# Kernel tuning notes

Hardware: AMD Instinct MI355X
Metric: run time of the kernel (lower is better)

Reference implementation:

```python
import jax, jax.numpy as jnp
import numpy as np

EPS = 1e-5

def _ln(x, g, b):
    mu = jnp.mean(x, axis=-1, keepdims=True)
    var = jnp.var(x, axis=-1, keepdims=True)
    return (x - mu) * jax.lax.rsqrt(var + EPS) * g + b

def setup_inputs() -> dict:
    key = jax.random.key(0)
    ks = jax.random.split(key, 8)
    B, N, D, H = 1, 512, 128, 128
    s = 1.0 / np.sqrt(D)
    inp = {
        'x': jax.random.normal(ks[0], (B, N, N, D), dtype=jnp.float32),
        'src_mask': jax.random.randint(ks[1], (B, N), 0, 2, dtype=jnp.int32),
        'ln_g': jnp.ones((D,), jnp.float32), 'ln_b': jnp.zeros((D,), jnp.float32),
        'Wl': jax.random.normal(ks[2], (D, H), jnp.float32) * s,
        'bl': jnp.zeros((H,), jnp.float32),
        'Wr': jax.random.normal(ks[3], (D, H), jnp.float32) * s,
        'br': jnp.zeros((H,), jnp.float32),
        # gates: faithful to nn.init.constant_(weight, 0.), constant_(bias, 1.)
        'Wlg': jnp.zeros((D, H), jnp.float32), 'blg': jnp.ones((H,), jnp.float32),
        'Wrg': jnp.zeros((D, H), jnp.float32), 'brg': jnp.ones((H,), jnp.float32),
        'Wog': jnp.zeros((D, H), jnp.float32), 'bog': jnp.ones((H,), jnp.float32),
        'oln_g': jnp.ones((H,), jnp.float32), 'oln_b': jnp.zeros((H,), jnp.float32),
        'Wo': jax.random.normal(ks[4], (H, D), jnp.float32) / np.sqrt(H),
        'bo': jnp.zeros((D,), jnp.float32),
    }
    return inp

def reference(x, src_mask, ln_g, ln_b, Wl, bl, Wr, br, Wlg, blg, Wrg, brg, Wog, bog, oln_g, oln_b, Wo, bo):
    # pairwise mask (B,i,j,1) = outer product of src_mask with itself
    m = src_mask.astype(jnp.float32)
    mask = (m[:, :, None] * m[:, None, :])[..., None]
    xn = _ln(x, ln_g, ln_b)
    # original applies left/right proj to detached xn (no grad to x via these paths)
    xd = jax.lax.stop_gradient(xn)
    left = (xd @ Wl + bl) * mask
    right = (xd @ Wr + br) * mask
    left = left * jax.nn.sigmoid(xn @ Wlg + blg)
    right = right * jax.nn.sigmoid(xn @ Wrg + brg)
    out_gate = jax.nn.sigmoid(xn @ Wog + bog)
    # ingoing mix: '... k j d, ... k i d -> ... i j d'
    out = jnp.einsum('bkjd,bkid->bijd', left, right)
    out = _ln(out, oln_g, oln_b) * out_gate
    return out @ Wo + bo
```

## Files before the change

kernel.cpp:

```cpp
#include <hip/hip_runtime.h>
#include <stdint.h>

#define NN 512
#define PP (NN * NN)

typedef __attribute__((ext_vector_type(8))) short bf16x8;
typedef __attribute__((ext_vector_type(4))) short bf16x4;
typedef __attribute__((ext_vector_type(4))) float f32x4;

#define MFMA16 __builtin_amdgcn_mfma_f32_16x16x32_bf16

__device__ __forceinline__ unsigned short f2bf(float f) {
  unsigned u = __float_as_uint(f);
  u += 0x7fffu + ((u >> 16) & 1u);
  return (unsigned short)(u >> 16);
}
__device__ __forceinline__ float bf2f(unsigned short s) {
  return __uint_as_float(((unsigned)s) << 16);
}
__device__ __forceinline__ unsigned pack2(float a, float b) {
  return (unsigned)f2bf(a) | ((unsigned)f2bf(b) << 16);
}
__device__ __forceinline__ float sigm(float t) { return 1.0f / (1.0f + __expf(-t)); }

__device__ __forceinline__ int sidx(int p, int h) {
  return p * 136 + (h ^ (((p >> 3) & 7) << 3));
}

__global__ __launch_bounds__(256) void k_prep(
    const float* __restrict__ w0, const float* __restrict__ w1,
    const float* __restrict__ w2, const float* __restrict__ w3,
    const float* __restrict__ w4, const float* __restrict__ w5,
    unsigned short* __restrict__ outw) {
  const float* src;
  switch (blockIdx.x) {
    case 0: src = w0; break; case 1: src = w1; break; case 2: src = w2; break;
    case 3: src = w3; break; case 4: src = w4; break; default: src = w5; break;
  }
  unsigned short* o = outw + blockIdx.x * 16384;
  for (int idx = threadIdx.x; idx < 16384; idx += 256) {
    int r = idx >> 7, c = idx & 127;
    o[idx] = f2bf(src[c * 128 + r]);
  }
}

__global__ __launch_bounds__(256) void k_ln(
    const float* __restrict__ x, const float* __restrict__ g,
    const float* __restrict__ b, unsigned short* __restrict__ xn) {
  const int lane = threadIdx.x & 63, wid = threadIdx.x >> 6;
  const int row = blockIdx.x * 32 + wid * 8 + (lane >> 3);
  const int ch = lane & 7;
  const float4* xr = (const float4*)(x + (size_t)row * 128 + ch * 16);
  float4 V[4];
  float s = 0.f, ss = 0.f;
#pragma unroll
  for (int q = 0; q < 4; ++q) {
    V[q] = xr[q];
    s  += V[q].x + V[q].y + V[q].z + V[q].w;
    ss += V[q].x * V[q].x + V[q].y * V[q].y + V[q].z * V[q].z + V[q].w * V[q].w;
  }
#pragma unroll
  for (int o = 1; o < 8; o <<= 1) { s += __shfl_xor(s, o); ss += __shfl_xor(ss, o); }
  float mu  = s * 0.0078125f;
  float var = ss * 0.0078125f - mu * mu;
  float rs  = rsqrtf(var + 1e-5f);
  const float4* gp = (const float4*)(g + ch * 16);
  const float4* bp = (const float4*)(b + ch * 16);
  unsigned pk[8];
#pragma unroll
  for (int q = 0; q < 4; ++q) {
    float4 vv = V[q], gg = gp[q], bb = bp[q];
    pk[2 * q]     = pack2((vv.x - mu) * rs * gg.x + bb.x, (vv.y - mu) * rs * gg.y + bb.y);
    pk[2 * q + 1] = pack2((vv.z - mu) * rs * gg.z + bb.z, (vv.w - mu) * rs * gg.w + bb.w);
  }
  unsigned short* dst = xn + (size_t)row * 128 + ch * 16;
  *(uint4*)dst       = make_uint4(pk[0], pk[1], pk[2], pk[3]);
  *(uint4*)(dst + 8) = make_uint4(pk[4], pk[5], pk[6], pk[7]);
}

__global__ __launch_bounds__(256) void k_proj(
    const unsigned short* __restrict__ xn,
    const unsigned short* __restrict__ WpT, const float* __restrict__ bp,
    const unsigned short* __restrict__ WgT, const float* __restrict__ bg,
    const int* __restrict__ mask,
    unsigned short* __restrict__ outb) {
  const int c  = blockIdx.y;
  const int k0 = blockIdx.x * 128;
  const int t = threadIdx.x, lane = t & 63, wid = t >> 6;
  const int wm = (wid >> 1) * 64, wn = (wid & 1) * 64;
  const int lr = lane & 15, lg = lane >> 4;
  __shared__ unsigned short sX[128 * 136];
  __shared__ unsigned short sW[128 * 136];

#pragma unroll
  for (int it = 0; it < 8; ++it) {
    int lin = it * 256 + t;
    int r = lin >> 4, ch = lin & 15;
    *(uint4*)&sX[r * 136 + ch * 8] =
        *(const uint4*)&xn[((size_t)(k0 + r) * NN + c) * 128 + ch * 8];
  }
#pragma unroll
  for (int it = 0; it < 8; ++it) {
    int lin = it * 256 + t;
    *(uint4*)&sW[(lin >> 4) * 136 + (lin & 15) * 8] = *(const uint4*)&WgT[lin * 8];
  }
  __syncthreads();

  f32x4 acc[4][4];
#pragma unroll
  for (int m = 0; m < 4; ++m)
#pragma unroll
    for (int n = 0; n < 4; ++n) { acc[m][n][0] = 0.f; acc[m][n][1] = 0.f; acc[m][n][2] = 0.f; acc[m][n][3] = 0.f; }

#pragma unroll
  for (int kk = 0; kk < 4; ++kk) {
    bf16x8 av[4], bv[4];
#pragma unroll
    for (int m = 0; m < 4; ++m)
      av[m] = *(const bf16x8*)&sW[(wm + m * 16 + lr) * 136 + kk * 32 + lg * 8];
#pragma unroll
    for (int n = 0; n < 4; ++n)
      bv[n] = *(const bf16x8*)&sX[(wn + n * 16 + lr) * 136 + kk * 32 + lg * 8];
#pragma unroll
    for (int m = 0; m < 4; ++m)
#pragma unroll
      for (int n = 0; n < 4; ++n)
        acc[m][n] = MFMA16(av[m], bv[n], acc[m][n], 0, 0, 0);
  }
  float sg[4][4][4];
#pragma unroll
  for (int m = 0; m < 4; ++m)
#pragma unroll
    for (int r = 0; r < 4; ++r) {
      int h = wm + m * 16 + lg * 4 + r;
      float bgv = bg[h];
#pragma unroll
      for (int n = 0; n < 4; ++n) sg[m][n][r] = sigm(acc[m][n][r] + bgv);
    }
  __syncthreads();
#pragma unroll
  for (int it = 0; it < 8; ++it) {
    int lin = it * 256 + t;
    *(uint4*)&sW[(lin >> 4) * 136 + (lin & 15) * 8] = *(const uint4*)&WpT[lin * 8];
  }
  __syncthreads();

#pragma unroll
  for (int m = 0; m < 4; ++m)
#pragma unroll
    for (int n = 0; n < 4; ++n) { acc[m][n][0] = 0.f; acc[m][n][1] = 0.f; acc[m][n][2] = 0.f; acc[m][n][3] = 0.f; }
#pragma unroll
  for (int kk = 0; kk < 4; ++kk) {
    bf16x8 av[4], bv[4];
#pragma unroll
    for (int m = 0; m < 4; ++m)
      av[m] = *(const bf16x8*)&sW[(wm + m * 16 + lr) * 136 + kk * 32 + lg * 8];
#pragma unroll
    for (int n = 0; n < 4; ++n)
      bv[n] = *(const bf16x8*)&sX[(wn + n * 16 + lr) * 136 + kk * 32 + lg * 8];
#pragma unroll
    for (int m = 0; m < 4; ++m)
#pragma unroll
      for (int n = 0; n < 4; ++n)
        acc[m][n] = MFMA16(av[m], bv[n], acc[m][n], 0, 0, 0);
  }

  const int maskc = mask[c];
  float mcol[4];
#pragma unroll
  for (int n = 0; n < 4; ++n)
    mcol[n] = (float)(maskc * mask[k0 + wn + n * 16 + lr]);
#pragma unroll
  for (int m = 0; m < 4; ++m)
#pragma unroll
    for (int r = 0; r < 4; ++r) {
      int h = wm + m * 16 + lg * 4 + r;
      float bpv = bp[h];
#pragma unroll
      for (int n = 0; n < 4; ++n) {
        float v = (acc[m][n][r] + bpv) * mcol[n] * sg[m][n][r];
        outb[(size_t)h * PP + (size_t)c * NN + k0 + wn + n * 16 + lr] = f2bf(v);
      }
    }
}

__global__ __launch_bounds__(512) void k_einsum(
    const unsigned short* __restrict__ rightT,
    const unsigned short* __restrict__ leftT,
    unsigned short* __restrict__ tmp) {
  const int bid = (blockIdx.x & 7) * 64 + (blockIdx.x >> 3);
  const int d = bid >> 2;
  const int i0 = ((bid >> 1) & 1) * 256, j0 = (bid & 1) * 256;
  const unsigned short* A = rightT + (size_t)d * PP;
  const unsigned short* B = leftT + (size_t)d * PP;
  const int t = threadIdx.x, lane = t & 63, wid = t >> 6;
  const int wm = (wid >> 2) * 128, wn = (wid & 3) * 64;
  const int lr = lane & 15, lg = lane >> 4;
  __shared__ unsigned short sA[256 * 72];
  __shared__ unsigned short sB[256 * 72];

  f32x4 acc[8][4];
#pragma unroll
  for (int m = 0; m < 8; ++m)
#pragma unroll
    for (int n = 0; n < 4; ++n) { acc[m][n][0] = 0.f; acc[m][n][1] = 0.f; acc[m][n][2] = 0.f; acc[m][n][3] = 0.f; }

  for (int kb = 0; kb < 8; ++kb) {
#pragma unroll
    for (int it = 0; it < 4; ++it) {
      int lin = it * 512 + t;
      int r = lin >> 3, ch = lin & 7;
      *(uint4*)&sA[r * 72 + ch * 8] =
          *(const uint4*)&A[(size_t)(i0 + r) * NN + kb * 64 + ch * 8];
      *(uint4*)&sB[r * 72 + ch * 8] =
          *(const uint4*)&B[(size_t)(j0 + r) * NN + kb * 64 + ch * 8];
    }
    __syncthreads();
#pragma unroll
    for (int kk = 0; kk < 2; ++kk) {
      bf16x8 bv[4];
#pragma unroll
      for (int n = 0; n < 4; ++n)
        bv[n] = *(const bf16x8*)&sB[(wn + n * 16 + lr) * 72 + kk * 32 + lg * 8];
#pragma unroll
      for (int m = 0; m < 8; ++m) {
        bf16x8 av = *(const bf16x8*)&sA[(wm + m * 16 + lr) * 72 + kk * 32 + lg * 8];
#pragma unroll
        for (int n = 0; n < 4; ++n)
          acc[m][n] = MFMA16(av, bv[n], acc[m][n], 0, 0, 0);
      }
    }
    __syncthreads();
  }
#pragma unroll
  for (int m = 0; m < 8; ++m)
#pragma unroll
    for (int r = 0; r < 4; ++r) {
      int row = wm + m * 16 + lg * 4 + r;
#pragma unroll
      for (int n = 0; n < 4; ++n) {
        int col = wn + n * 16 + lr;
        tmp[(size_t)d * PP + (size_t)(i0 + row) * NN + j0 + col] = f2bf(acc[m][n][r]);
      }
    }
}

__global__ __launch_bounds__(512, 4) void k_final(
    const unsigned short* __restrict__ xn,
    const unsigned short* __restrict__ WogT, const float* __restrict__ bog,
    const unsigned short* __restrict__ WoT, const float* __restrict__ bo,
    const unsigned short* __restrict__ tmp,
    const float* __restrict__ og, const float* __restrict__ ob,
    float* __restrict__ out) {
  const int p0 = blockIdx.x * 128;
  const int t = threadIdx.x, lane = t & 63, wid = t >> 6;
  const int wm = (wid >> 2) * 64, wn = (wid & 3) * 32;
  const int lr = lane & 15, lg = lane >> 4;
  __shared__ unsigned short sT[128 * 136];
  __shared__ unsigned short sSig[128 * 136];

  {
    const int ps = t & 15;
    const int hb = ((t >> 4) & 15) * 8 + (t >> 8) * 4;
    uint4 a[4];
#pragma unroll
    for (int e = 0; e < 4; ++e)
      a[e] = *(const uint4*)&tmp[(size_t)(hb + e) * PP + p0 + 8 * ps];
#pragma unroll
    for (int r = 0; r < 8; ++r) {
      bf16x4 y;
#pragma unroll
      for (int e = 0; e < 4; ++e) {
        unsigned w = ((const unsigned*)&a[e])[r >> 1];
        y[e] = (short)((r & 1) ? (w >> 16) : (w & 0xffffu));
      }
      *(bf16x4*)&sT[sidx(8 * ps + r, hb)] = y;
    }
  }

  f32x4 acc[4][2];
#pragma unroll
  for (int m = 0; m < 4; ++m)
#pragma unroll
    for (int n = 0; n < 2; ++n) { acc[m][n][0] = 0.f; acc[m][n][1] = 0.f; acc[m][n][2] = 0.f; acc[m][n][3] = 0.f; }
#pragma unroll
  for (int kk = 0; kk < 4; ++kk) {
    bf16x8 av[4], bv[2];
#pragma unroll
    for (int m = 0; m < 4; ++m)
      av[m] = *(const bf16x8*)&xn[(size_t)(p0 + wm + m * 16 + lr) * 128 + kk * 32 + lg * 8];
#pragma unroll
    for (int n = 0; n < 2; ++n)
      bv[n] = *(const bf16x8*)&WogT[(wn + n * 16 + lr) * 128 + kk * 32 + lg * 8];
#pragma unroll
    for (int m = 0; m < 4; ++m)
#pragma unroll
      for (int n = 0; n < 2; ++n)
        acc[m][n] = MFMA16(av[m], bv[n], acc[m][n], 0, 0, 0);
  }
  float bogv[2];
#pragma unroll
  for (int n = 0; n < 2; ++n) bogv[n] = bog[wn + n * 16 + lr];
#pragma unroll
  for (int m = 0; m < 4; ++m)
#pragma unroll
    for (int r = 0; r < 4; ++r) {
      int p = wm + m * 16 + lg * 4 + r;
#pragma unroll
      for (int n = 0; n < 2; ++n)
        sSig[sidx(p, wn + n * 16 + lr)] = f2bf(sigm(acc[m][n][r] + bogv[n]));
    }
  __syncthreads();

  {
    const int p = t >> 2, q = t & 3;
    bf16x8 tv[4];
    float s = 0.f, ss = 0.f;
#pragma unroll
    for (int c = 0; c < 4; ++c) {
      tv[c] = *(const bf16x8*)&sT[sidx(p, q * 32 + c * 8)];
#pragma unroll
      for (int e = 0; e < 8; ++e) {
        float f = bf2f((unsigned short)tv[c][e]);
        s += f; ss += f * f;
      }
    }
    s += __shfl_xor(s, 1); ss += __shfl_xor(ss, 1);
    s += __shfl_xor(s, 2); ss += __shfl_xor(ss, 2);
    float mu = s * 0.0078125f;
    float var = ss * 0.0078125f - mu * mu;
    float rs = rsqrtf(var + 1e-5f);
#pragma unroll
    for (int c = 0; c < 4; ++c) {
      int h0 = q * 32 + c * 8;
      float4 og0 = *(const float4*)&og[h0], og1 = *(const float4*)&og[h0 + 4];
      float4 ob0 = *(const float4*)&ob[h0], ob1 = *(const float4*)&ob[h0 + 4];
      float ogv[8] = {og0.x, og0.y, og0.z, og0.w, og1.x, og1.y, og1.z, og1.w};
      float obv[8] = {ob0.x, ob0.y, ob0.z, ob0.w, ob1.x, ob1.y, ob1.z, ob1.w};
      bf16x8 gv = *(const bf16x8*)&sSig[sidx(p, h0)];
      bf16x8 y;
#pragma unroll
      for (int e = 0; e < 8; ++e) {
        float alpha = rs * ogv[e];
        float beta = fmaf(-mu, alpha, obv[e]);
        float yf = fmaf(bf2f((unsigned short)tv[c][e]), alpha, beta) *
                   bf2f((unsigned short)gv[e]);
        y[e] = (short)f2bf(yf);
      }
      *(bf16x8*)&sT[sidx(p, h0)] = y;
    }
  }
  __syncthreads();

#pragma unroll
  for (int m = 0; m < 4; ++m)
#pragma unroll
    for (int n = 0; n < 2; ++n) { acc[m][n][0] = 0.f; acc[m][n][1] = 0.f; acc[m][n][2] = 0.f; acc[m][n][3] = 0.f; }
#pragma unroll
  for (int kk = 0; kk < 4; ++kk) {
    const int h0 = kk * 32 + lg * 8;
    bf16x8 av[4], bv[2];
#pragma unroll
    for (int m = 0; m < 4; ++m)
      av[m] = *(const bf16x8*)&sT[sidx(wm + m * 16 + lr, h0)];
#pragma unroll
    for (int n = 0; n < 2; ++n)
      bv[n] = *(const bf16x8*)&WoT[(wn + n * 16 + lr) * 128 + h0];
#pragma unroll
    for (int m = 0; m < 4; ++m)
#pragma unroll
      for (int n = 0; n < 2; ++n)
        acc[m][n] = MFMA16(av[m], bv[n], acc[m][n], 0, 0, 0);
  }

  float bov[2];
#pragma unroll
  for (int n = 0; n < 2; ++n) bov[n] = bo[wn + n * 16 + lr];
#pragma unroll
  for (int m = 0; m < 4; ++m)
#pragma unroll
    for (int r = 0; r < 4; ++r) {
      int p = wm + m * 16 + lg * 4 + r;
#pragma unroll
      for (int n = 0; n < 2; ++n)
        out[(size_t)(p0 + p) * 128 + wn + n * 16 + lr] = acc[m][n][r] + bov[n];
    }
}

extern "C" void kernel_launch(void* const* d_in, const int* in_sizes, int n_in,
                              void* d_out, int out_size, void* d_ws, size_t ws_size,
                              hipStream_t stream) {
  (void)in_sizes; (void)n_in; (void)out_size;
  const float* x    = (const float*)d_in[0];
  const int*   msk  = (const int*)d_in[1];
  const float* ln_g = (const float*)d_in[2];
  const float* ln_b = (const float*)d_in[3];
  const float* Wl   = (const float*)d_in[4];
  const float* bl   = (const float*)d_in[5];
  const float* Wr   = (const float*)d_in[6];
  const float* br   = (const float*)d_in[7];
  const float* Wlg  = (const float*)d_in[8];
  const float* blg  = (const float*)d_in[9];
  const float* Wrg  = (const float*)d_in[10];
  const float* brg  = (const float*)d_in[11];
  const float* Wog  = (const float*)d_in[12];
  const float* bog  = (const float*)d_in[13];
  const float* olng = (const float*)d_in[14];
  const float* olnb = (const float*)d_in[15];
  const float* Wo   = (const float*)d_in[16];
  const float* bo   = (const float*)d_in[17];
  float* out = (float*)d_out;

  const size_t need = (1ull << 20) + 4ull * (1ull << 26);
  if (ws_size < need) return;
  char* ws = (char*)d_ws;
  unsigned short* wT    = (unsigned short*)ws;
  unsigned short* xn    = (unsigned short*)(ws + (1ull << 20));
  unsigned short* leftT = (unsigned short*)(ws + (1ull << 20) + (1ull << 26));
  unsigned short* rightT= (unsigned short*)(ws + (1ull << 20) + (2ull << 26));
  unsigned short* tmp   = (unsigned short*)(ws + (1ull << 20) + (3ull << 26));

  hipLaunchKernelGGL(k_prep, dim3(6), dim3(256), 0, stream, Wl, Wr, Wlg, Wrg, Wog, Wo, wT);
  hipLaunchKernelGGL(k_ln, dim3(PP / 32), dim3(256), 0, stream, x, ln_g, ln_b, xn);
  hipLaunchKernelGGL(k_proj, dim3(4, NN), dim3(256), 0, stream,
                     xn, wT + 0 * 16384, bl, wT + 2 * 16384, blg, msk, leftT);
  hipLaunchKernelGGL(k_proj, dim3(4, NN), dim3(256), 0, stream,
                     xn, wT + 1 * 16384, br, wT + 3 * 16384, brg, msk, rightT);
  hipLaunchKernelGGL(k_einsum, dim3(512), dim3(512), 0, stream, rightT, leftT, tmp);
  hipLaunchKernelGGL(k_final, dim3(PP / 128), dim3(512), 0, stream,
                     xn, wT + 4 * 16384, bog, wT + 5 * 16384, bo, tmp, olng, olnb, out);
}
```

Before: 305.7 us.

## Restructure final kernel so each wave owns 16 rows, keeping the gate in registers

Rewrites k_final so each wave owns 16 pair rows across all 128 channels. The out-gate GEMM is computed transposed so the sigmoid values stay in registers, and the LayerNorm, gating and Wo GEMM are fused in registers through cross-lane shuffles. This removes the sSig shared buffer, one __syncthreads and a shared-memory round trip for the normalized activations. Blocks shrink to 64 rows and 256 threads, which raises register pressure and changes occupancy, and the shuffle-based lane remapping is intricate and could be wrong.

```diff
diff --git a/kernel.cpp b/kernel.cpp
--- a/kernel.cpp
+++ b/kernel.cpp
@@ -22,6 +22,15 @@
   return (unsigned)f2bf(a) | ((unsigned)f2bf(b) << 16);
 }
 __device__ __forceinline__ float sigm(float t) { return 1.0f / (1.0f + __expf(-t)); }
+
+__device__ __forceinline__ f32x4 shflx4(f32x4 v, int m) {
+  f32x4 r;
+  r[0] = __shfl_xor(v[0], m);
+  r[1] = __shfl_xor(v[1], m);
+  r[2] = __shfl_xor(v[2], m);
+  r[3] = __shfl_xor(v[3], m);
+  return r;
+}
 
 __device__ __forceinline__ int sidx(int p, int h) {
   return p * 136 + (h ^ (((p >> 3) & 7) << 3));
@@ -245,23 +254,21 @@
     }
 }
 
-__global__ __launch_bounds__(512, 4) void k_final(
+__global__ __launch_bounds__(256, 3) void k_final(
     const unsigned short* __restrict__ xn,
     const unsigned short* __restrict__ WogT, const float* __restrict__ bog,
     const unsigned short* __restrict__ WoT, const float* __restrict__ bo,
     const unsigned short* __restrict__ tmp,
     const float* __restrict__ og, const float* __restrict__ ob,
     float* __restrict__ out) {
-  const int p0 = blockIdx.x * 128;
+  const int p0 = blockIdx.x * 64;
   const int t = threadIdx.x, lane = t & 63, wid = t >> 6;
-  const int wm = (wid >> 2) * 64, wn = (wid & 3) * 32;
   const int lr = lane & 15, lg = lane >> 4;
-  __shared__ unsigned short sT[128 * 136];
-  __shared__ unsigned short sSig[128 * 136];
+  __shared__ unsigned short sT[64 * 136];
 
   {
-    const int ps = t & 15;
-    const int hb = ((t >> 4) & 15) * 8 + (t >> 8) * 4;
+    const int ps = t & 7;
+    const int hb = (t >> 3) * 4;
     uint4 a[4];
 #pragma unroll
     for (int e = 0; e < 4; ++e)
@@ -278,113 +285,96 @@
     }
   }
 
-  f32x4 acc[4][2];
-#pragma unroll
-  for (int m = 0; m < 4; ++m)
-#pragma unroll
-    for (int n = 0; n < 2; ++n) { acc[m][n][0] = 0.f; acc[m][n][1] = 0.f; acc[m][n][2] = 0.f; acc[m][n][3] = 0.f; }
+  const int prow = p0 + wid * 16 + lr;
+
+  f32x4 acc1[8];
+#pragma unroll
+  for (int m = 0; m < 8; ++m) { acc1[m][0] = 0.f; acc1[m][1] = 0.f; acc1[m][2] = 0.f; acc1[m][3] = 0.f; }
 #pragma unroll
   for (int kk = 0; kk < 4; ++kk) {
-    bf16x8 av[4], bv[2];
-#pragma unroll
-    for (int m = 0; m < 4; ++m)
-      av[m] = *(const bf16x8*)&xn[(size_t)(p0 + wm + m * 16 + lr) * 128 + kk * 32 + lg * 8];
-#pragma unroll
-    for (int n = 0; n < 2; ++n)
-      bv[n] = *(const bf16x8*)&WogT[(wn + n * 16 + lr) * 128 + kk * 32 + lg * 8];
-#pragma unroll
-    for (int m = 0; m < 4; ++m)
-#pragma unroll
-      for (int n = 0; n < 2; ++n)
-        acc[m][n] = MFMA16(av[m], bv[n], acc[m][n], 0, 0, 0);
-  }
-  float bogv[2];
-#pragma unroll
-  for (int n = 0; n < 2; ++n) bogv[n] = bog[wn + n * 16 + lr];
-#pragma unroll
-  for (int m = 0; m < 4; ++m)
+    bf16x8 bvx = *(const bf16x8*)&xn[(size_t)prow * 128 + kk * 32 + lg * 8];
+#pragma unroll
+    for (int m = 0; m < 8; ++m) {
+      bf16x8 av = *(const bf16x8*)&WogT[(m * 16 + lr) * 128 + kk * 32 + lg * 8];
+      acc1[m] = MFMA16(av, bvx, acc1[m], 0, 0, 0);
+    }
+  }
+  f32x4 sigv[8];
+#pragma unroll
+  for (int m = 0; m < 8; ++m) {
+    float4 b4 = *(const float4*)&bog[m * 16 + lg * 4];
+    sigv[m][0] = sigm(acc1[m][0] + b4.x);
+    sigv[m][1] = sigm(acc1[m][1] + b4.y);
+    sigv[m][2] = sigm(acc1[m][2] + b4.z);
+    sigv[m][3] = sigm(acc1[m][3] + b4.w);
+  }
+
+  __syncthreads();
+
+  bf16x8 tv[4];
+  float s = 0.f, ss = 0.f;
+#pragma unroll
+  for (int kk = 0; kk < 4; ++kk) {
+    tv[kk] = *(const bf16x8*)&sT[sidx(wid * 16 + lr, kk * 32 + lg * 8)];
+#pragma unroll
+    for (int e = 0; e < 8; ++e) {
+      float f = bf2f((unsigned short)tv[kk][e]);
+      s += f; ss += f * f;
+    }
+  }
+  s += __shfl_xor(s, 16); ss += __shfl_xor(ss, 16);
+  s += __shfl_xor(s, 32); ss += __shfl_xor(ss, 32);
+  const float mu = s * 0.0078125f;
+  const float rs = rsqrtf(ss * 0.0078125f - mu * mu + 1e-5f);
+
+  f32x4 acc2[8];
+#pragma unroll
+  for (int n = 0; n < 8; ++n) { acc2[n][0] = 0.f; acc2[n][1] = 0.f; acc2[n][2] = 0.f; acc2[n][3] = 0.f; }
+#pragma unroll
+  for (int kk = 0; kk < 4; ++kk) {
+    f32x4 w1 = (lg & 2) ? sigv[2 * kk + 1] : sigv[2 * kk];
+    f32x4 w2 = (lg & 2) ? sigv[2 * kk] : sigv[2 * kk + 1];
+    f32x4 r16 = shflx4(w1, 16);
+    f32x4 r32 = shflx4(w2, 32);
+    f32x4 r48 = shflx4(w2, 48);
+    f32x4 h0v = (lg == 0) ? sigv[2 * kk]
+              : (lg == 1) ? r48
+              : (lg == 2) ? r32 : r16;
+    f32x4 h1v = (lg == 3) ? sigv[2 * kk + 1]
+              : (lg == 0) ? r16
+              : (lg == 1) ? r32 : r48;
+
+    const int h0 = kk * 32 + lg * 8;
+    float4 og0 = *(const float4*)&og[h0], og1 = *(const float4*)&og[h0 + 4];
+    float4 ob0 = *(const float4*)&ob[h0], ob1 = *(const float4*)&ob[h0 + 4];
+    float ogv[8] = {og0.x, og0.y, og0.z, og0.w, og1.x, og1.y, og1.z, og1.w};
+    float obv[8] = {ob0.x, ob0.y, ob0.z, ob0.w, ob1.x, ob1.y, ob1.z, ob1.w};
+    float sgv[8] = {h0v[0], h0v[1], h0v[2], h0v[3], h1v[0], h1v[1], h1v[2], h1v[3]};
+
+    bf16x8 yv;
+#pragma unroll
+    for (int e = 0; e < 8; ++e) {
+      float alpha = rs * ogv[e];
+      float beta = fmaf(-mu, alpha, obv[e]);
+      float yf = fmaf(bf2f((unsigned short)tv[kk][e]), alpha, beta) * sgv[e];
+      yv[e] = (short)f2bf(yf);
+    }
+#pragma unroll
+    for (int n = 0; n < 8; ++n) {
+      bf16x8 bv = *(const bf16x8*)&WoT[(n * 16 + lr) * 128 + h0];
+      acc2[n] = MFMA16(yv, bv, acc2[n], 0, 0, 0);
+    }
+  }
+
+#pragma unroll
+  for (int n = 0; n < 8; ++n) {
+    float bov = bo[n * 16 + lr];
 #pragma unroll
     for (int r = 0; r < 4; ++r) {
-      int p = wm + m * 16 + lg * 4 + r;
-#pragma unroll
-      for (int n = 0; n < 2; ++n)
-        sSig[sidx(p, wn + n * 16 + lr)] = f2bf(sigm(acc[m][n][r] + bogv[n]));
-    }
-  __syncthreads();
-
-  {
-    const int p = t >> 2, q = t & 3;
-    bf16x8 tv[4];
-    float s = 0.f, ss = 0.f;
-#pragma unroll
-    for (int c = 0; c < 4; ++c) {
-      tv[c] = *(const bf16x8*)&sT[sidx(p, q * 32 + c * 8)];
-#pragma unroll
-      for (int e = 0; e < 8; ++e) {
-        float f = bf2f((unsigned short)tv[c][e]);
-        s += f; ss += f * f;
-      }
-    }
-    s += __shfl_xor(s, 1); ss += __shfl_xor(ss, 1);
-    s += __shfl_xor(s, 2); ss += __shfl_xor(ss, 2);
-    float mu = s * 0.0078125f;
-    float var = ss * 0.0078125f - mu * mu;
-    float rs = rsqrtf(var + 1e-5f);
-#pragma unroll
-    for (int c = 0; c < 4; ++c) {
-      int h0 = q * 32 + c * 8;
-      float4 og0 = *(const float4*)&og[h0], og1 = *(const float4*)&og[h0 + 4];
-      float4 ob0 = *(const float4*)&ob[h0], ob1 = *(const float4*)&ob[h0 + 4];
-      float ogv[8] = {og0.x, og0.y, og0.z, og0.w, og1.x, og1.y, og1.z, og1.w};
-      float obv[8] = {ob0.x, ob0.y, ob0.z, ob0.w, ob1.x, ob1.y, ob1.z, ob1.w};
-      bf16x8 gv = *(const bf16x8*)&sSig[sidx(p, h0)];
-      bf16x8 y;
-#pragma unroll
-      for (int e = 0; e < 8; ++e) {
-        float alpha = rs * ogv[e];
-        float beta = fmaf(-mu, alpha, obv[e]);
-        float yf = fmaf(bf2f((unsigned short)tv[c][e]), alpha, beta) *
-                   bf2f((unsigned short)gv[e]);
-        y[e] = (short)f2bf(yf);
-      }
-      *(bf16x8*)&sT[sidx(p, h0)] = y;
-    }
-  }
-  __syncthreads();
-
-#pragma unroll
-  for (int m = 0; m < 4; ++m)
-#pragma unroll
-    for (int n = 0; n < 2; ++n) { acc[m][n][0] = 0.f; acc[m][n][1] = 0.f; acc[m][n][2] = 0.f; acc[m][n][3] = 0.f; }
-#pragma unroll
-  for (int kk = 0; kk < 4; ++kk) {
-    const int h0 = kk * 32 + lg * 8;
-    bf16x8 av[4], bv[2];
-#pragma unroll
-    for (int m = 0; m < 4; ++m)
-      av[m] = *(const bf16x8*)&sT[sidx(wm + m * 16 + lr, h0)];
-#pragma unroll
-    for (int n = 0; n < 2; ++n)
-      bv[n] = *(const bf16x8*)&WoT[(wn + n * 16 + lr) * 128 + h0];
-#pragma unroll
-    for (int m = 0; m < 4; ++m)
-#pragma unroll
-      for (int n = 0; n < 2; ++n)
-        acc[m][n] = MFMA16(av[m], bv[n], acc[m][n], 0, 0, 0);
-  }
-
-  float bov[2];
-#pragma unroll
-  for (int n = 0; n < 2; ++n) bov[n] = bo[wn + n * 16 + lr];
-#pragma unroll
-  for (int m = 0; m < 4; ++m)
-#pragma unroll
-    for (int r = 0; r < 4; ++r) {
-      int p = wm + m * 16 + lg * 4 + r;
-#pragma unroll
-      for (int n = 0; n < 2; ++n)
-        out[(size_t)(p0 + p) * 128 + wn + n * 16 + lr] = acc[m][n][r] + bov[n];
-    }
+      int p = p0 + wid * 16 + lg * 4 + r;
+      out[(size_t)p * 128 + n * 16 + lr] = acc2[n][r] + bov;
+    }
+  }
 }
 
 extern "C" void kernel_launch(void* const* d_in, const int* in_sizes, int n_in,
@@ -427,6 +417,6 @@
   hipLaunchKernelGGL(k_proj, dim3(4, NN), dim3(256), 0, stream,
                      xn, wT + 1 * 16384, br, wT + 3 * 16384, brg, msk, rightT);
   hipLaunchKernelGGL(k_einsum, dim3(512), dim3(512), 0, stream, rightT, leftT, tmp);
-  hipLaunchKernelGGL(k_final, dim3(PP / 128), dim3(512), 0, stream,
+  hipLaunchKernelGGL(k_final, dim3(PP / 64), dim3(256), 0, stream,
                      xn, wT + 4 * 16384, bog, wT + 5 * 16384, bo, tmp, olng, olnb, out);
 }
```

Measured after the change: 347.2 us. +13.6%, slower.
